# Performance work log

Hardware: AMD Instinct MI355X
Metric: run time of the kernel (lower is better)

The kernel has to match this reference:

```python
import jax, jax.numpy as jnp
import numpy as np
import math

B, C, H, W = 8, 64, 256, 256
E, NH = 256, 8
HD = E // NH  # 32


def get_coords(h, w):
    xx, yy = jnp.meshgrid(jnp.arange(h, dtype=jnp.float32), jnp.arange(w, dtype=jnp.float32), indexing='ij')
    return jnp.stack((xx.reshape(-1), yy.reshape(-1)), axis=-1)  # [N, 2]


def setup_inputs() -> dict:
    key = jax.random.key(0)
    ks = jax.random.split(key, 12)
    def xavier(k, shape):
        fan_out, fan_in = shape
        a = math.sqrt(6.0 / (fan_in + fan_out))
        return jax.random.uniform(k, shape, jnp.float32, -a, a)
    x = jax.random.normal(ks[0], (B, C, H, W), jnp.float32)
    z = jax.random.normal(ks[1], (B, C), jnp.float32)
    pos = jax.random.uniform(ks[2], (B, NH, 2), jnp.float32) * (H - 1)
    Wq = xavier(ks[3], (E, C)); bq = jnp.zeros((E,), jnp.float32)
    Wk = xavier(ks[4], (E, C)); bk = jnp.zeros((E,), jnp.float32)
    Wv = xavier(ks[5], (E, C)); bv = jnp.zeros((E,), jnp.float32)
    Wp = xavier(ks[6], (HD, 2)); bp = jax.random.uniform(ks[7], (HD,), jnp.float32, -1.0, 1.0) / math.sqrt(2.0)
    return {"x": x, "z": z, "pos": pos, "Wq": Wq, "bq": bq, "Wk": Wk, "bk": bk,
            "Wv": Wv, "bv": bv, "Wp": Wp, "bp": bp}


def reference(x, z, pos, Wq, bq, Wk, bk, Wv, bv, Wp, bp):
    b, c, h, w = x.shape
    n = h * w
    x_flat = x.reshape(b, c, n).transpose(0, 2, 1)          # [B, N, C]
    pos_grid = get_coords(h, w)                              # [N, 2]
    q = (z @ Wq.T + bq).reshape(b, NH, HD)                   # [B, H, hd]
    k = (x_flat @ Wk.T + bk).reshape(b, n, NH, HD)           # [B, N, H, hd]
    # relative-position modulation of keys
    rel = pos_grid[None, :, None, :] - pos[:, None, :, :]    # [B, N, H, 2]
    qxk = rel @ Wp.T + bp                                    # [B, N, H, hd]
    k = k * qxk
    v = x_flat @ Wv.T + bv                                   # [B, N, E]
    attn_logits = jnp.einsum('bhc,bnhc->bnh', q, k) / math.sqrt(HD)
    attention = jax.nn.softmax(attn_logits, axis=1)          # softmax over N
    pos_out = jnp.einsum('bnh,nx->bhx', attention, pos_grid) # [B, H, 2]
    values = jnp.einsum('bnh,bnc->bhc', attention, v)        # [B, H, E]
    return (values, pos_out)
```

## Files before the change

kernel.cpp:

```cpp
#include <hip/hip_runtime.h>

#define NN    65536
#define NSUB  256
#define NBLK  (NN/NSUB)

typedef short bf16x8 __attribute__((ext_vector_type(8)));
typedef float f32x4v __attribute__((ext_vector_type(4)));
typedef unsigned short ushort_t;
typedef unsigned int uint_t;

#define XSTR   72
#define XHI_B  0
#define XLO_B  36864
#define LGA_B  36864
#define LGSTR  28
#define RED_B  73728
#define SMEM_BYTES 74240

#define WTHI_B  0
#define WTLO_B  32768
#define CJ_B    65536
#define PM_B    66304
#define PL_B    131840
#define PSP_B   197376
#define PSX_B   328448
#define Q_B     4522752
#define QSTR    68

__device__ __forceinline__ uint_t bf16_rne_bits(float f) {
  uint_t u = __float_as_uint(f);
  return (u + 0x7FFFu + ((u >> 16) & 1u)) >> 16;
}
template <int CTRL>
__device__ __forceinline__ float dpp_add(float x) {
  int t = __builtin_amdgcn_update_dpp(0, __float_as_int(x), CTRL, 0xf, 0xf, false);
  return x + __int_as_float(t);
}
template <int CTRL>
__device__ __forceinline__ float dpp_maxs(float x) {
  int t = __builtin_amdgcn_update_dpp((int)0xFF800000u, __float_as_int(x), CTRL, 0xf, 0xf, false);
  return fmaxf(x, __int_as_float(t));
}
__device__ __forceinline__ float wave_sum(float x) {
  x = dpp_add<0x111>(x); x = dpp_add<0x112>(x); x = dpp_add<0x114>(x);
  x = dpp_add<0x118>(x); x = dpp_add<0x142>(x); x = dpp_add<0x143>(x);
  return __int_as_float(__builtin_amdgcn_readlane(__float_as_int(x), 63));
}
__device__ __forceinline__ float wave_max(float x) {
  x = dpp_maxs<0x111>(x); x = dpp_maxs<0x112>(x); x = dpp_maxs<0x114>(x);
  x = dpp_maxs<0x118>(x); x = dpp_maxs<0x142>(x); x = dpp_maxs<0x143>(x);
  return __int_as_float(__builtin_amdgcn_readlane(__float_as_int(x), 63));
}

__global__ __launch_bounds__(64) void prep_kernel(
    const float* __restrict__ z,  const float* __restrict__ Wq, const float* __restrict__ bq,
    const float* __restrict__ Wk, const float* __restrict__ bk,
    const float* __restrict__ Wp, const float* __restrict__ bp,
    ushort_t* __restrict__ WThi, ushort_t* __restrict__ WTlo, float* __restrict__ Cj)
{
  const int h = blockIdx.x, b = blockIdx.y, t = threadIdx.x;
  __shared__ float q[32];
  if (t < 32) {
    const int e = h*32 + t;
    float a = bq[e];
    const float* zr = z + b*64;
    const float* wr = Wq + e*64;
    #pragma unroll 8
    for (int c = 0; c < 64; ++c) a += zr[c]*wr[c];
    q[t] = a;
  }
  __syncthreads();
  const int c = t;
  float w[3] = {0.f, 0.f, 0.f};
  #pragma unroll 4
  for (int hd = 0; hd < 32; ++hd) {
    const float qk = q[hd] * Wk[(h*32+hd)*64 + c];
    w[0] += qk * bp[hd];
    w[1] += qk * Wp[hd*2+0];
    w[2] += qk * Wp[hd*2+1];
  }
  #pragma unroll
  for (int j = 0; j < 3; ++j) {
    const int coeff = h*3 + j;
    const uint_t hb = bf16_rne_bits(w[j]);
    const float  fh = __uint_as_float(hb << 16);
    const uint_t lb = bf16_rne_bits(w[j] - fh);
    WThi[(b*32 + coeff)*64 + c] = (ushort_t)hb;
    WTlo[(b*32 + coeff)*64 + c] = (ushort_t)lb;
  }
  if (h == 0) {
    #pragma unroll
    for (int r = 0; r < 8; ++r) {
      WThi[(b*32 + 24 + r)*64 + c] = 0;
      WTlo[(b*32 + 24 + r)*64 + c] = 0;
    }
  }
  if (t < 3) {
    float s = 0.f;
    for (int hd = 0; hd < 32; ++hd) {
      const float m = (t == 0) ? bp[hd] : Wp[hd*2 + (t-1)];
      s += q[hd] * m * bk[h*32+hd];
    }
    Cj[b*24 + h*3 + t] = s;
  }
}

__global__ __launch_bounds__(256, 2) void main_kernel(
    const float* __restrict__ x, const float* __restrict__ pos,
    const ushort_t* __restrict__ WThi, const ushort_t* __restrict__ WTlo,
    const float* __restrict__ Cj,
    float* __restrict__ Pm, float* __restrict__ Pl,
    float* __restrict__ Psp, float* __restrict__ Psx)
{
  extern __shared__ char smc[];
  ushort_t* xhi = (ushort_t*)(smc + XHI_B);
  ushort_t* xlo = (ushort_t*)(smc + XLO_B);
  float*    lga = (float*)(smc + LGA_B);
  float*    red = (float*)(smc + RED_B);
  const int t   = threadIdx.x;
  const int blk = blockIdx.x;
  const int b   = blockIdx.y;
  const int n0  = blk * NSUB;
  const int wid = t >> 6, lid = t & 63;
  const int c0  = lid & 15, q4 = lid >> 4;

  bf16x8 bh[2][2], bl[2][2];
  {
    const ushort_t* wtb_h = WThi + b*2048;
    const ushort_t* wtb_l = WTlo + b*2048;
    #pragma unroll
    for (int nt = 0; nt < 2; ++nt)
      #pragma unroll
      for (int ks = 0; ks < 2; ++ks) {
        const int off = (nt*16 + c0)*64 + ks*32 + q4*8;
        bh[nt][ks] = *(const bf16x8*)(wtb_h + off);
        bl[nt][ks] = *(const bf16x8*)(wtb_l + off);
      }
  }

  {
    const float* xg = x + (size_t)b*64*NN + n0 + t;
    #pragma unroll
    for (int cc = 0; cc < 4; ++cc) {
      float v[16];
      #pragma unroll
      for (int i = 0; i < 16; ++i) v[i] = xg[(size_t)(cc*16+i)*NN];
      uint_t hb[16], lb[16];
      #pragma unroll
      for (int i = 0; i < 16; ++i) {
        hb[i] = bf16_rne_bits(v[i]);
        lb[i] = bf16_rne_bits(v[i] - __uint_as_float(hb[i] << 16));
      }
      uint4 H0 = make_uint4(hb[0]|(hb[1]<<16), hb[2]|(hb[3]<<16), hb[4]|(hb[5]<<16), hb[6]|(hb[7]<<16));
      uint4 H1 = make_uint4(hb[8]|(hb[9]<<16), hb[10]|(hb[11]<<16), hb[12]|(hb[13]<<16), hb[14]|(hb[15]<<16));
      uint4 L0 = make_uint4(lb[0]|(lb[1]<<16), lb[2]|(lb[3]<<16), lb[4]|(lb[5]<<16), lb[6]|(lb[7]<<16));
      uint4 L1 = make_uint4(lb[8]|(lb[9]<<16), lb[10]|(lb[11]<<16), lb[12]|(lb[13]<<16), lb[14]|(lb[15]<<16));
      char* dh = smc + XHI_B + t*144 + cc*32;
      char* dl = smc + XLO_B + t*144 + cc*32;
      *(uint4*)(dh)      = H0;  *(uint4*)(dh + 16) = H1;
      *(uint4*)(dl)      = L0;  *(uint4*)(dl + 16) = L1;
    }
  }

  float cj[24];
  {
    const float* cjp = Cj + b*24;
    #pragma unroll
    for (int k = 0; k < 24; ++k) cj[k] = cjp[k];
  }
  float rxh[8], py[8];
  #pragma unroll
  for (int h = 0; h < 8; ++h) {
    rxh[h] = (float)blk - pos[(b*8+h)*2 + 0];
    py[h]  = pos[(b*8+h)*2 + 1];
  }

  __syncthreads();

  f32x4v acc[4][2];
  #pragma unroll
  for (int mt = 0; mt < 4; ++mt) { acc[mt][0] = (f32x4v)0.f; acc[mt][1] = (f32x4v)0.f; }
  {
    const int mrow0 = wid*64;
    #pragma unroll
    for (int mt = 0; mt < 4; ++mt) {
      const int row = mrow0 + mt*16 + c0;
      const ushort_t* ph = xhi + row*XSTR + q4*8;
      const ushort_t* pl = xlo + row*XSTR + q4*8;
      bf16x8 ah0 = *(const bf16x8*)(ph);
      bf16x8 ah1 = *(const bf16x8*)(ph + 32);
      bf16x8 al0 = *(const bf16x8*)(pl);
      bf16x8 al1 = *(const bf16x8*)(pl + 32);
      #pragma unroll
      for (int nt = 0; nt < 2; ++nt) {
        f32x4v a = acc[mt][nt];
        a = __builtin_amdgcn_mfma_f32_16x16x32_bf16(ah0, bh[nt][0], a, 0, 0, 0);
        a = __builtin_amdgcn_mfma_f32_16x16x32_bf16(ah1, bh[nt][1], a, 0, 0, 0);
        a = __builtin_amdgcn_mfma_f32_16x16x32_bf16(ah0, bl[nt][0], a, 0, 0, 0);
        a = __builtin_amdgcn_mfma_f32_16x16x32_bf16(ah1, bl[nt][1], a, 0, 0, 0);
        a = __builtin_amdgcn_mfma_f32_16x16x32_bf16(al0, bh[nt][0], a, 0, 0, 0);
        a = __builtin_amdgcn_mfma_f32_16x16x32_bf16(al1, bh[nt][1], a, 0, 0, 0);
        acc[mt][nt] = a;
      }
    }
  }
  __syncthreads();

  {
    const int mrow0 = wid*64;
    #pragma unroll
    for (int mt = 0; mt < 4; ++mt)
      #pragma unroll
      for (int r = 0; r < 4; ++r) {
        const int prow = mrow0 + mt*16 + q4*4 + r;
        lga[prow*LGSTR + c0] = acc[mt][0][r];
        if (c0 < 8) lga[prow*LGSTR + 16 + c0] = acc[mt][1][r];
      }
  }
  __syncthreads();

  float a24[24];
  {
    const float4* ap = (const float4*)(lga + t*LGSTR);
    #pragma unroll
    for (int r = 0; r < 6; ++r) *(float4*)(a24 + 4*r) = ap[r];
  }
  const float tf = (float)t;
  float lg[8];
  #pragma unroll
  for (int h = 0; h < 8; ++h) {
    const float a0 = a24[h*3+0] + cj[h*3+0];
    const float a1 = a24[h*3+1] + cj[h*3+1];
    const float a2 = a24[h*3+2] + cj[h*3+2];
    lg[h] = (a0 + rxh[h]*a1 + (tf - py[h])*a2) * 0.17677669529663687f;
  }

  #pragma unroll
  for (int h = 0; h < 8; ++h) {
    const float m = wave_max(lg[h]);
    if (lid == 0) red[h*4 + wid] = m;
  }
  __syncthreads();

  float p[8];
  #pragma unroll
  for (int h = 0; h < 8; ++h) {
    const float M = fmaxf(fmaxf(red[h*4+0], red[h*4+1]), fmaxf(red[h*4+2], red[h*4+3]));
    p[h] = __expf(lg[h] - M);
  }
  #pragma unroll
  for (int h = 0; h < 8; ++h) {
    const float sp  = wave_sum(p[h]);
    const float spj = wave_sum(p[h] * tf);
    if (lid == 0) { red[32 + h*4 + wid] = sp; red[64 + h*4 + wid] = spj; }
  }
  __syncthreads();

  if (t < 8) {
    const int base = (b*NBLK + blk)*8 + t;
    const float M = fmaxf(fmaxf(red[t*4+0], red[t*4+1]), fmaxf(red[t*4+2], red[t*4+3]));
    const float L  = red[32+t*4+0] + red[32+t*4+1] + red[32+t*4+2] + red[32+t*4+3];
    const float SJ = red[64+t*4+0] + red[64+t*4+1] + red[64+t*4+2] + red[64+t*4+3];
    Pm[base] = M;
    Pl[base] = L;
    Psp[base*2+0] = (float)blk * L;
    Psp[base*2+1] = SJ;
  }

  float aB[8];
  #pragma unroll
  for (int h = 0; h < 8; ++h) aB[h] = 0.f;
  {
    const ushort_t* xrow = xhi + (wid*64)*XSTR + lid;
    #pragma unroll 8
    for (int j = 0; j < 64; ++j) {
      const float xv = __uint_as_float(((uint_t)xrow[j*XSTR]) << 16);
      #pragma unroll
      for (int h = 0; h < 8; ++h) {
        const float pj = __int_as_float(__builtin_amdgcn_readlane(__float_as_int(p[h]), j));
        aB[h] = fmaf(pj, xv, aB[h]);
      }
    }
  }
  __syncthreads();
  {
    float* pstage = (float*)smc;
    #pragma unroll
    for (int h = 0; h < 8; ++h) pstage[(wid*8 + h)*64 + lid] = aB[h];
  }
  __syncthreads();
  {
    const float* pstage = (const float*)smc;
    const size_t pb = ((size_t)(b*NBLK + blk))*8;
    #pragma unroll
    for (int r = 0; r < 2; ++r) {
      const int idx = t + 256*r;
      const float s = pstage[idx] + pstage[512+idx] + pstage[1024+idx] + pstage[1536+idx];
      Psx[pb*64 + idx] = s;
    }
  }
}

__global__ __launch_bounds__(256) void reduce1_kernel(
    const float* __restrict__ Pm, const float* __restrict__ Pl,
    const float* __restrict__ Psp, const float* __restrict__ Psx,
    float* __restrict__ Q)
{
  const int g = blockIdx.x, h = blockIdx.y, b = blockIdx.z, t = threadIdx.x;
  __shared__ float al[32];
  __shared__ float mgs;
  __shared__ float sums[3];
  __shared__ float sxl[256];
  const int base = (b*NBLK + g*32)*8 + h;

  float m_t = -1e30f;
  if (t < 32) m_t = Pm[base + t*8];
  if (t < 64) {
    float mm = m_t;
    #pragma unroll
    for (int off = 16; off >= 1; off >>= 1) mm = fmaxf(mm, __shfl_xor(mm, off, 64));
    if (t == 0) mgs = mm;
  }
  __syncthreads();
  const float Mg = mgs;
  if (t < 32) {
    const float a = __expf(m_t - Mg);
    al[t] = a;
    float lt = Pl[base + t*8] * a;
    float sx = Psp[(base + t*8)*2 + 0] * a;
    float sy = Psp[(base + t*8)*2 + 1] * a;
    #pragma unroll
    for (int off = 16; off >= 1; off >>= 1) {
      lt += __shfl_xor(lt, off, 64);
      sx += __shfl_xor(sx, off, 64);
      sy += __shfl_xor(sy, off, 64);
    }
    if (t == 0) { sums[0] = lt; sums[1] = sx; sums[2] = sy; }
  }
  __syncthreads();
  {
    const int c = t & 63, g2 = t >> 6;
    float acc = 0.f;
    #pragma unroll
    for (int i = 0; i < 8; ++i) {
      const int k = g2*8 + i;
      acc += al[k] * Psx[(size_t)(base + k*8)*64 + c];
    }
    sxl[g2*64 + c] = acc;
  }
  __syncthreads();
  float* q = Q + ((b*8 + h)*8 + g)*QSTR;
  if (t < 64) q[4+t] = sxl[t] + sxl[64+t] + sxl[128+t] + sxl[192+t];
  if (t == 0) { q[0] = Mg; q[1] = sums[0]; q[2] = sums[1]; q[3] = sums[2]; }
}

__global__ __launch_bounds__(64) void reduce2_kernel(
    const float* __restrict__ Q, const float* __restrict__ Wv, const float* __restrict__ bv,
    float* __restrict__ out)
{
  const int h = blockIdx.x, b = blockIdx.y, t = threadIdx.x;
  __shared__ float qm[8], bl[8], l8[8], sx8[8], sy8[8];
  __shared__ float SXs[64];
  const float* qb = Q + ((b*8 + h)*8)*QSTR;

  if (t < 8) qm[t] = qb[t*QSTR + 0];
  __syncthreads();
  float M = qm[0];
  #pragma unroll
  for (int g = 1; g < 8; ++g) M = fmaxf(M, qm[g]);
  if (t < 8) {
    const float be = __expf(qm[t] - M);
    bl[t]  = be;
    l8[t]  = be * qb[t*QSTR + 1];
    sx8[t] = be * qb[t*QSTR + 2];
    sy8[t] = be * qb[t*QSTR + 3];
  }
  __syncthreads();
  float L = 0.f;
  #pragma unroll
  for (int g = 0; g < 8; ++g) L += l8[g];
  const float invL = 1.0f / L;
  {
    float s = 0.f;
    #pragma unroll
    for (int g = 0; g < 8; ++g) s += bl[g] * qb[g*QSTR + 4 + t];
    SXs[t] = s * invL;
  }
  __syncthreads();

  #pragma unroll
  for (int r = 0; r < 4; ++r) {
    const int e = t + 64*r;
    float v = bv[e];
    const float* wvr = Wv + e*64;
    #pragma unroll 8
    for (int c = 0; c < 64; ++c) v += wvr[c] * SXs[c];
    out[(b*8 + h)*256 + e] = v;
  }
  if (t == 0) {
    float spx = 0.f, spy = 0.f;
    #pragma unroll
    for (int g = 0; g < 8; ++g) { spx += sx8[g]; spy += sy8[g]; }
    out[16384 + (b*8 + h)*2 + 0] = spx * invL;
    out[16384 + (b*8 + h)*2 + 1] = spy * invL;
  }
}

extern "C" void kernel_launch(void* const* d_in, const int* in_sizes, int n_in,
                              void* d_out, int out_size, void* d_ws, size_t ws_size,
                              hipStream_t stream)
{
  const float* x   = (const float*)d_in[0];
  const float* z   = (const float*)d_in[1];
  const float* pos = (const float*)d_in[2];
  const float* Wq  = (const float*)d_in[3];
  const float* bq  = (const float*)d_in[4];
  const float* Wk  = (const float*)d_in[5];
  const float* bk  = (const float*)d_in[6];
  const float* Wv  = (const float*)d_in[7];
  const float* bv  = (const float*)d_in[8];
  const float* Wp  = (const float*)d_in[9];
  const float* bp  = (const float*)d_in[10];
  float* out = (float*)d_out;
  char*  wsb = (char*)d_ws;

  ushort_t* WThi = (ushort_t*)(wsb + WTHI_B);
  ushort_t* WTlo = (ushort_t*)(wsb + WTLO_B);
  float* Cj  = (float*)(wsb + CJ_B);
  float* Pm  = (float*)(wsb + PM_B);
  float* Pl  = (float*)(wsb + PL_B);
  float* Psp = (float*)(wsb + PSP_B);
  float* Psx = (float*)(wsb + PSX_B);
  float* Q   = (float*)(wsb + Q_B);

  (void)hipFuncSetAttribute((const void*)main_kernel,
                            hipFuncAttributeMaxDynamicSharedMemorySize, SMEM_BYTES);

  prep_kernel   <<<dim3(8,8),    64,  0,          stream>>>(z, Wq, bq, Wk, bk, Wp, bp, WThi, WTlo, Cj);
  main_kernel   <<<dim3(NBLK,8), 256, SMEM_BYTES, stream>>>(x, pos, WThi, WTlo, Cj, Pm, Pl, Psp, Psx);
  reduce1_kernel<<<dim3(8,8,8),  256, 0,          stream>>>(Pm, Pl, Psp, Psx, Q);
  reduce2_kernel<<<dim3(8,8),    64,  0,          stream>>>(Q, Wv, bv, out);
}
```

Before: 247.8 us.

## Halve main kernel tile to 128 positions per block with 128 threads

```diff
diff --git a/kernel.cpp b/kernel.cpp
--- a/kernel.cpp
+++ b/kernel.cpp
@@ -1,7 +1,7 @@
 #include <hip/hip_runtime.h>
 
 #define NN    65536
-#define NSUB  256
+#define NSUB  128
 #define NBLK  (NN/NSUB)
 
 typedef short bf16x8 __attribute__((ext_vector_type(8)));
@@ -11,20 +11,20 @@
 
 #define XSTR   72
 #define XHI_B  0
-#define XLO_B  36864
-#define LGA_B  36864
+#define XLO_B  18432
+#define LGA_B  18432
 #define LGSTR  28
-#define RED_B  73728
-#define SMEM_BYTES 74240
+#define RED_B  36864
+#define SMEM_BYTES 37056
 
 #define WTHI_B  0
 #define WTLO_B  32768
 #define CJ_B    65536
 #define PM_B    66304
-#define PL_B    131840
-#define PSP_B   197376
-#define PSX_B   328448
-#define Q_B     4522752
+#define PL_B    197376
+#define PSP_B   328448
+#define PSX_B   590592
+#define Q_B     8979200
 #define QSTR    68
 
 __device__ __forceinline__ uint_t bf16_rne_bits(float f) {
@@ -105,7 +105,7 @@
   }
 }
 
-__global__ __launch_bounds__(256, 2) void main_kernel(
+__global__ __launch_bounds__(128, 2) void main_kernel(
     const float* __restrict__ x, const float* __restrict__ pos,
     const ushort_t* __restrict__ WThi, const ushort_t* __restrict__ WTlo,
     const float* __restrict__ Cj,
@@ -114,7 +114,6 @@
 {
   extern __shared__ char smc[];
   ushort_t* xhi = (ushort_t*)(smc + XHI_B);
-  ushort_t* xlo = (ushort_t*)(smc + XLO_B);
   float*    lga = (float*)(smc + LGA_B);
   float*    red = (float*)(smc + RED_B);
   const int t   = threadIdx.x;
@@ -141,24 +140,29 @@
   {
     const float* xg = x + (size_t)b*64*NN + n0 + t;
     #pragma unroll
-    for (int cc = 0; cc < 4; ++cc) {
-      float v[16];
-      #pragma unroll
-      for (int i = 0; i < 16; ++i) v[i] = xg[(size_t)(cc*16+i)*NN];
-      uint_t hb[16], lb[16];
-      #pragma unroll
-      for (int i = 0; i < 16; ++i) {
-        hb[i] = bf16_rne_bits(v[i]);
-        lb[i] = bf16_rne_bits(v[i] - __uint_as_float(hb[i] << 16));
+    for (int half = 0; half < 2; ++half) {
+      float v[32];
+      #pragma unroll
+      for (int i = 0; i < 32; ++i) v[i] = xg[(size_t)(half*32+i)*NN];
+      #pragma unroll
+      for (int cc2 = 0; cc2 < 2; ++cc2) {
+        const int cc = half*2 + cc2;
+        uint_t hb[16], lb[16];
+        #pragma unroll
+        for (int i = 0; i < 16; ++i) {
+          const float f = v[cc2*16+i];
+          hb[i] = bf16_rne_bits(f);
+          lb[i] = bf16_rne_bits(f - __uint_as_float(hb[i] << 16));
+        }
+        uint4 H0 = make_uint4(hb[0]|(hb[1]<<16), hb[2]|(hb[3]<<16), hb[4]|(hb[5]<<16), hb[6]|(hb[7]<<16));
+        uint4 H1 = make_uint4(hb[8]|(hb[9]<<16), hb[10]|(hb[11]<<16), hb[12]|(hb[13]<<16), hb[14]|(hb[15]<<16));
+        uint4 L0 = make_uint4(lb[0]|(lb[1]<<16), lb[2]|(lb[3]<<16), lb[4]|(lb[5]<<16), lb[6]|(lb[7]<<16));
+        uint4 L1 = make_uint4(lb[8]|(lb[9]<<16), lb[10]|(lb[11]<<16), lb[12]|(lb[13]<<16), lb[14]|(lb[15]<<16));
+        char* dh = smc + XHI_B + t*144 + cc*32;
+        char* dl = smc + XLO_B + t*144 + cc*32;
+        *(uint4*)(dh)      = H0;  *(uint4*)(dh + 16) = H1;
+        *(uint4*)(dl)      = L0;  *(uint4*)(dl + 16) = L1;
       }
-      uint4 H0 = make_uint4(hb[0]|(hb[1]<<16), hb[2]|(hb[3]<<16), hb[4]|(hb[5]<<16), hb[6]|(hb[7]<<16));
-      uint4 H1 = make_uint4(hb[8]|(hb[9]<<16), hb[10]|(hb[11]<<16), hb[12]|(hb[13]<<16), hb[14]|(hb[15]<<16));
-      uint4 L0 = make_uint4(lb[0]|(lb[1]<<16), lb[2]|(lb[3]<<16), lb[4]|(lb[5]<<16), lb[6]|(lb[7]<<16));
-      uint4 L1 = make_uint4(lb[8]|(lb[9]<<16), lb[10]|(lb[11]<<16), lb[12]|(lb[13]<<16), lb[14]|(lb[15]<<16));
-      char* dh = smc + XHI_B + t*144 + cc*32;
-      char* dl = smc + XLO_B + t*144 + cc*32;
-      *(uint4*)(dh)      = H0;  *(uint4*)(dh + 16) = H1;
-      *(uint4*)(dl)      = L0;  *(uint4*)(dl + 16) = L1;
     }
   }
 
@@ -168,10 +172,11 @@
     #pragma unroll
     for (int k = 0; k < 24; ++k) cj[k] = cjp[k];
   }
+  const int gx = blk >> 1;
   float rxh[8], py[8];
   #pragma unroll
   for (int h = 0; h < 8; ++h) {
-    rxh[h] = (float)blk - pos[(b*8+h)*2 + 0];
+    rxh[h] = (float)gx - pos[(b*8+h)*2 + 0];
     py[h]  = pos[(b*8+h)*2 + 1];
   }
 
@@ -186,7 +191,7 @@
     for (int mt = 0; mt < 4; ++mt) {
       const int row = mrow0 + mt*16 + c0;
       const ushort_t* ph = xhi + row*XSTR + q4*8;
-      const ushort_t* pl = xlo + row*XSTR + q4*8;
+      const ushort_t* pl = (ushort_t*)(smc + XLO_B) + row*XSTR + q4*8;
       bf16x8 ah0 = *(const bf16x8*)(ph);
       bf16x8 ah1 = *(const bf16x8*)(ph + 32);
       bf16x8 al0 = *(const bf16x8*)(pl);
@@ -225,7 +230,7 @@
     #pragma unroll
     for (int r = 0; r < 6; ++r) *(float4*)(a24 + 4*r) = ap[r];
   }
-  const float tf = (float)t;
+  const float tf = (float)(((blk & 1) << 7) + t);
   float lg[8];
   #pragma unroll
   for (int h = 0; h < 8; ++h) {
@@ -238,32 +243,32 @@
   #pragma unroll
   for (int h = 0; h < 8; ++h) {
     const float m = wave_max(lg[h]);
-    if (lid == 0) red[h*4 + wid] = m;
+    if (lid == 0) red[h*2 + wid] = m;
   }
   __syncthreads();
 
   float p[8];
   #pragma unroll
   for (int h = 0; h < 8; ++h) {
-    const float M = fmaxf(fmaxf(red[h*4+0], red[h*4+1]), fmaxf(red[h*4+2], red[h*4+3]));
+    const float M = fmaxf(red[h*2+0], red[h*2+1]);
     p[h] = __expf(lg[h] - M);
   }
   #pragma unroll
   for (int h = 0; h < 8; ++h) {
     const float sp  = wave_sum(p[h]);
     const float spj = wave_sum(p[h] * tf);
-    if (lid == 0) { red[32 + h*4 + wid] = sp; red[64 + h*4 + wid] = spj; }
+    if (lid == 0) { red[16 + h*2 + wid] = sp; red[32 + h*2 + wid] = spj; }
   }
   __syncthreads();
 
   if (t < 8) {
     const int base = (b*NBLK + blk)*8 + t;
-    const float M = fmaxf(fmaxf(red[t*4+0], red[t*4+1]), fmaxf(red[t*4+2], red[t*4+3]));
-    const float L  = red[32+t*4+0] + red[32+t*4+1] + red[32+t*4+2] + red[32+t*4+3];
-    const float SJ = red[64+t*4+0] + red[64+t*4+1] + red[64+t*4+2] + red[64+t*4+3];
+    const float M  = fmaxf(red[t*2+0], red[t*2+1]);
+    const float L  = red[16+t*2+0] + red[16+t*2+1];
+    const float SJ = red[32+t*2+0] + red[32+t*2+1];
     Pm[base] = M;
     Pl[base] = L;
-    Psp[base*2+0] = (float)blk * L;
+    Psp[base*2+0] = (float)gx * L;
     Psp[base*2+1] = SJ;
   }
 
@@ -293,9 +298,9 @@
     const float* pstage = (const float*)smc;
     const size_t pb = ((size_t)(b*NBLK + blk))*8;
     #pragma unroll
-    for (int r = 0; r < 2; ++r) {
-      const int idx = t + 256*r;
-      const float s = pstage[idx] + pstage[512+idx] + pstage[1024+idx] + pstage[1536+idx];
+    for (int r = 0; r < 4; ++r) {
+      const int idx = t + 128*r;
+      const float s = pstage[idx] + pstage[512+idx];
       Psx[pb*64 + idx] = s;
     }
   }
@@ -307,30 +312,30 @@
     float* __restrict__ Q)
 {
   const int g = blockIdx.x, h = blockIdx.y, b = blockIdx.z, t = threadIdx.x;
-  __shared__ float al[32];
+  __shared__ float al[64];
   __shared__ float mgs;
   __shared__ float sums[3];
   __shared__ float sxl[256];
-  const int base = (b*NBLK + g*32)*8 + h;
+  const int base = (b*NBLK + g*64)*8 + h;
 
   float m_t = -1e30f;
-  if (t < 32) m_t = Pm[base + t*8];
   if (t < 64) {
+    m_t = Pm[base + t*8];
     float mm = m_t;
     #pragma unroll
-    for (int off = 16; off >= 1; off >>= 1) mm = fmaxf(mm, __shfl_xor(mm, off, 64));
+    for (int off = 32; off >= 1; off >>= 1) mm = fmaxf(mm, __shfl_xor(mm, off, 64));
     if (t == 0) mgs = mm;
   }
   __syncthreads();
   const float Mg = mgs;
-  if (t < 32) {
+  if (t < 64) {
     const float a = __expf(m_t - Mg);
     al[t] = a;
     float lt = Pl[base + t*8] * a;
     float sx = Psp[(base + t*8)*2 + 0] * a;
     float sy = Psp[(base + t*8)*2 + 1] * a;
     #pragma unroll
-    for (int off = 16; off >= 1; off >>= 1) {
+    for (int off = 32; off >= 1; off >>= 1) {
       lt += __shfl_xor(lt, off, 64);
       sx += __shfl_xor(sx, off, 64);
       sy += __shfl_xor(sy, off, 64);
@@ -342,8 +347,8 @@
     const int c = t & 63, g2 = t >> 6;
     float acc = 0.f;
     #pragma unroll
-    for (int i = 0; i < 8; ++i) {
-      const int k = g2*8 + i;
+    for (int i = 0; i < 16; ++i) {
+      const int k = g2*16 + i;
       acc += al[k] * Psx[(size_t)(base + k*8)*64 + c];
     }
     sxl[g2*64 + c] = acc;
@@ -433,11 +438,8 @@
   float* Psx = (float*)(wsb + PSX_B);
   float* Q   = (float*)(wsb + Q_B);
 
-  (void)hipFuncSetAttribute((const void*)main_kernel,
-                            hipFuncAttributeMaxDynamicSharedMemorySize, SMEM_BYTES);
-
   prep_kernel   <<<dim3(8,8),    64,  0,          stream>>>(z, Wq, bq, Wk, bk, Wp, bp, WThi, WTlo, Cj);
-  main_kernel   <<<dim3(NBLK,8), 256, SMEM_BYTES, stream>>>(x, pos, WThi, WTlo, Cj, Pm, Pl, Psp, Psx);
+  main_kernel   <<<dim3(NBLK,8), 128, SMEM_BYTES, stream>>>(x, pos, WThi, WTlo, Cj, Pm, Pl, Psp, Psx);
   reduce1_kernel<<<dim3(8,8,8),  256, 0,          stream>>>(Pm, Pl, Psp, Psx, Q);
   reduce2_kernel<<<dim3(8,8),    64,  0,          stream>>>(Q, Wv, bv, out);
 }
```

Result: slower. 253.8 us (+2.4%).

## Compute softmax-weighted x sums with MFMA and vectorize x load conversion

Applied to the files above, without the earlier changes.

```diff
diff --git a/kernel.cpp b/kernel.cpp
--- a/kernel.cpp
+++ b/kernel.cpp
@@ -14,22 +14,28 @@
 #define XLO_B  36864
 #define LGA_B  36864
 #define LGSTR  28
+#define PSTR   264
 #define RED_B  73728
-#define SMEM_BYTES 74240
+#define SMEM_BYTES 74112
 
 #define WTHI_B  0
 #define WTLO_B  32768
 #define CJ_B    65536
 #define PM_B    66304
-#define PL_B    131840
-#define PSP_B   197376
-#define PSX_B   328448
-#define Q_B     4522752
+#define PL_B    197376
+#define PSP_B   328448
+#define PSX_B   590592
+#define Q_B     8979200
 #define QSTR    68
 
 __device__ __forceinline__ uint_t bf16_rne_bits(float f) {
   uint_t u = __float_as_uint(f);
   return (u + 0x7FFFu + ((u >> 16) & 1u)) >> 16;
+}
+__device__ __forceinline__ uint_t cvt_pk_bf16(float a, float b) {
+  uint_t r;
+  asm("v_cvt_pk_bf16_f32 %0, %1, %2" : "=v"(r) : "v"(a), "v"(b));
+  return r;
 }
 template <int CTRL>
 __device__ __forceinline__ float dpp_add(float x) {
@@ -114,7 +120,6 @@
 {
   extern __shared__ char smc[];
   ushort_t* xhi = (ushort_t*)(smc + XHI_B);
-  ushort_t* xlo = (ushort_t*)(smc + XLO_B);
   float*    lga = (float*)(smc + LGA_B);
   float*    red = (float*)(smc + RED_B);
   const int t   = threadIdx.x;
@@ -139,26 +144,31 @@
   }
 
   {
-    const float* xg = x + (size_t)b*64*NN + n0 + t;
-    #pragma unroll
-    for (int cc = 0; cc < 4; ++cc) {
-      float v[16];
+    const float* xg = x + (size_t)b*64*NN + (size_t)(wid*16)*NN + n0 + 4*lid;
+    f32x4v v[16];
+    #pragma unroll
+    for (int c = 0; c < 16; ++c) v[c] = *(const f32x4v*)(xg + (size_t)c*NN);
+    #pragma unroll
+    for (int i = 0; i < 4; ++i) {
+      uint_t H[8], L[8];
       #pragma unroll
-      for (int i = 0; i < 16; ++i) v[i] = xg[(size_t)(cc*16+i)*NN];
-      uint_t hb[16], lb[16];
-      #pragma unroll
-      for (int i = 0; i < 16; ++i) {
-        hb[i] = bf16_rne_bits(v[i]);
-        lb[i] = bf16_rne_bits(v[i] - __uint_as_float(hb[i] << 16));
+      for (int jp = 0; jp < 8; ++jp) {
+        const float f0 = v[2*jp][i], f1 = v[2*jp+1][i];
+        const uint_t hpk = cvt_pk_bf16(f0, f1);
+        const float h0 = __uint_as_float(hpk << 16);
+        const float h1 = __uint_as_float(hpk & 0xFFFF0000u);
+        const uint_t l0 = __float_as_uint(f0 - h0);
+        const uint_t l1 = __float_as_uint(f1 - h1);
+        H[jp] = hpk;
+        L[jp] = __builtin_amdgcn_perm(l1, l0, 0x07060302u);
       }
-      uint4 H0 = make_uint4(hb[0]|(hb[1]<<16), hb[2]|(hb[3]<<16), hb[4]|(hb[5]<<16), hb[6]|(hb[7]<<16));
-      uint4 H1 = make_uint4(hb[8]|(hb[9]<<16), hb[10]|(hb[11]<<16), hb[12]|(hb[13]<<16), hb[14]|(hb[15]<<16));
-      uint4 L0 = make_uint4(lb[0]|(lb[1]<<16), lb[2]|(lb[3]<<16), lb[4]|(lb[5]<<16), lb[6]|(lb[7]<<16));
-      uint4 L1 = make_uint4(lb[8]|(lb[9]<<16), lb[10]|(lb[11]<<16), lb[12]|(lb[13]<<16), lb[14]|(lb[15]<<16));
-      char* dh = smc + XHI_B + t*144 + cc*32;
-      char* dl = smc + XLO_B + t*144 + cc*32;
-      *(uint4*)(dh)      = H0;  *(uint4*)(dh + 16) = H1;
-      *(uint4*)(dl)      = L0;  *(uint4*)(dl + 16) = L1;
+      const int row = 4*lid + i;
+      char* dh = smc + XHI_B + row*144 + wid*32;
+      char* dl = smc + XLO_B + row*144 + wid*32;
+      *(uint4*)(dh)      = make_uint4(H[0], H[1], H[2], H[3]);
+      *(uint4*)(dh + 16) = make_uint4(H[4], H[5], H[6], H[7]);
+      *(uint4*)(dl)      = make_uint4(L[0], L[1], L[2], L[3]);
+      *(uint4*)(dl + 16) = make_uint4(L[4], L[5], L[6], L[7]);
     }
   }
 
@@ -186,7 +196,7 @@
     for (int mt = 0; mt < 4; ++mt) {
       const int row = mrow0 + mt*16 + c0;
       const ushort_t* ph = xhi + row*XSTR + q4*8;
-      const ushort_t* pl = xlo + row*XSTR + q4*8;
+      const ushort_t* pl = (ushort_t*)(smc + XLO_B) + row*XSTR + q4*8;
       bf16x8 ah0 = *(const bf16x8*)(ph);
       bf16x8 ah1 = *(const bf16x8*)(ph + 32);
       bf16x8 al0 = *(const bf16x8*)(pl);
@@ -248,6 +258,19 @@
     const float M = fmaxf(fmaxf(red[h*4+0], red[h*4+1]), fmaxf(red[h*4+2], red[h*4+3]));
     p[h] = __expf(lg[h] - M);
   }
+
+  {
+    ushort_t* pls = (ushort_t*)(smc + LGA_B);
+    #pragma unroll
+    for (int h = 0; h < 8; ++h) {
+      const uint_t hb = bf16_rne_bits(p[h]);
+      const float  hf = __uint_as_float(hb << 16);
+      const uint_t lb = __float_as_uint(p[h] - hf) >> 16;
+      pls[h*PSTR + t]     = (ushort_t)hb;
+      pls[(h+8)*PSTR + t] = (ushort_t)lb;
+    }
+  }
+
   #pragma unroll
   for (int h = 0; h < 8; ++h) {
     const float sp  = wave_sum(p[h]);
@@ -258,7 +281,7 @@
 
   if (t < 8) {
     const int base = (b*NBLK + blk)*8 + t;
-    const float M = fmaxf(fmaxf(red[t*4+0], red[t*4+1]), fmaxf(red[t*4+2], red[t*4+3]));
+    const float M  = fmaxf(fmaxf(red[t*4+0], red[t*4+1]), fmaxf(red[t*4+2], red[t*4+3]));
     const float L  = red[32+t*4+0] + red[32+t*4+1] + red[32+t*4+2] + red[32+t*4+3];
     const float SJ = red[64+t*4+0] + red[64+t*4+1] + red[64+t*4+2] + red[64+t*4+3];
     Pm[base] = M;
@@ -267,36 +290,32 @@
     Psp[base*2+1] = SJ;
   }
 
-  float aB[8];
-  #pragma unroll
-  for (int h = 0; h < 8; ++h) aB[h] = 0.f;
-  {
-    const ushort_t* xrow = xhi + (wid*64)*XSTR + lid;
-    #pragma unroll 8
-    for (int j = 0; j < 64; ++j) {
-      const float xv = __uint_as_float(((uint_t)xrow[j*XSTR]) << 16);
+  {
+    const ushort_t* pls = (const ushort_t*)(smc + LGA_B);
+    bf16x8 afr[8];
+    #pragma unroll
+    for (int ks = 0; ks < 8; ++ks)
+      afr[ks] = *(const bf16x8*)(pls + c0*PSTR + ks*32 + q4*8);
+
+    f32x4v accB = (f32x4v)0.f;
+    const int ch = wid*16 + c0;
+    #pragma unroll
+    for (int ks = 0; ks < 8; ++ks) {
+      const ushort_t* xcol = xhi + (ks*32 + q4*8)*XSTR + ch;
+      bf16x8 bfr;
       #pragma unroll
-      for (int h = 0; h < 8; ++h) {
-        const float pj = __int_as_float(__builtin_amdgcn_readlane(__float_as_int(p[h]), j));
-        aB[h] = fmaf(pj, xv, aB[h]);
+      for (int j = 0; j < 8; ++j) bfr[j] = (short)xcol[j*XSTR];
+      accB = __builtin_amdgcn_mfma_f32_16x16x32_bf16(afr[ks], bfr, accB, 0, 0, 0);
+    }
+
+    const size_t pb64 = ((size_t)(b*NBLK + blk))*8*64;
+    #pragma unroll
+    for (int r = 0; r < 4; ++r) {
+      const float o = __shfl_xor(accB[r], 32, 64);
+      if (q4 < 2) {
+        const int h = q4*4 + r;
+        Psx[pb64 + h*64 + ch] = accB[r] + o;
       }
-    }
-  }
-  __syncthreads();
-  {
-    float* pstage = (float*)smc;
-    #pragma unroll
-    for (int h = 0; h < 8; ++h) pstage[(wid*8 + h)*64 + lid] = aB[h];
-  }
-  __syncthreads();
-  {
-    const float* pstage = (const float*)smc;
-    const size_t pb = ((size_t)(b*NBLK + blk))*8;
-    #pragma unroll
-    for (int r = 0; r < 2; ++r) {
-      const int idx = t + 256*r;
-      const float s = pstage[idx] + pstage[512+idx] + pstage[1024+idx] + pstage[1536+idx];
-      Psx[pb*64 + idx] = s;
     }
   }
 }
```

Result: faster. 238.2 us (-3.9%).
